# Performance work log

Measured on AMD Instinct MI355X. Metric: run time of the kernel, lower is better.

Reference implementation:

```python
import jax, jax.numpy as jnp
import numpy as np

B, S, E = 1, 4096, 2048
H, HK, D = 16, 4, 128  # num_heads, num_kv_heads, head_dim


def setup_inputs() -> dict:
    key = jax.random.key(0)
    ks = jax.random.split(key, 5)
    sc = 0.02
    return {
        "x": jax.random.normal(ks[0], (B, S, E), dtype=jnp.float32),
        "Wq": jax.random.normal(ks[1], (H * D, E), dtype=jnp.float32) * sc,
        "Wk": jax.random.normal(ks[2], (HK * D, E), dtype=jnp.float32) * sc,
        "Wv": jax.random.normal(ks[3], (HK * D, E), dtype=jnp.float32) * sc,
        "Wo": jax.random.normal(ks[4], (E, H * D), dtype=jnp.float32) * sc,
    }


def reference(x, Wq, Wk, Wv, Wo):
    b, s, _ = x.shape
    # projections (bias=False Linear: x @ W.T), split heads, [B, H, S, D]
    q = (x @ Wq.T).reshape(b, s, H, D).transpose(0, 2, 1, 3).astype(jnp.float16)
    k = (x @ Wk.T).reshape(b, s, HK, D).transpose(0, 2, 1, 3).astype(jnp.float16)
    v = (x @ Wv.T).reshape(b, s, HK, D).transpose(0, 2, 1, 3).astype(jnp.float16)
    # GQA: repeat_interleave kv heads to match query heads
    rep = H // HK
    k = jnp.repeat(k, rep, axis=1)
    v = jnp.repeat(v, rep, axis=1)
    # SDPA in fp32 (non-causal), result cast to half as in torch code
    qf, kf, vf = q.astype(jnp.float32), k.astype(jnp.float32), v.astype(jnp.float32)
    scores = jnp.einsum("bhsd,bhtd->bhst", qf, kf) / np.float32(np.sqrt(D))
    attn = jax.nn.softmax(scores, axis=-1)
    out = jnp.einsum("bhst,bhtd->bhsd", attn, vf).astype(jnp.float16)
    # merge heads and output projection in fp32
    out = out.transpose(0, 2, 1, 3).reshape(b, s, H * D).astype(jnp.float32)
    return out @ Wo.T
```

## Files before the change

### kernel.cpp

```cpp
#include <hip/hip_runtime.h>
#include <stdint.h>

#define SEQ 4096
#define EMB 2048
#define NH 16
#define HDIM 128

typedef _Float16 f16;
typedef _Float16 f16x2 __attribute__((ext_vector_type(2)));
typedef _Float16 f16x4 __attribute__((ext_vector_type(4)));
typedef _Float16 f16x8 __attribute__((ext_vector_type(8)));
typedef float f32x4 __attribute__((ext_vector_type(4)));
typedef unsigned u32x2 __attribute__((ext_vector_type(2)));

#define MFMA16(a, b, c) __builtin_amdgcn_mfma_f32_16x16x32_f16((a), (b), (c), 0, 0, 0)

#define OFF_XH   0ull
#define OFF_WCAT 8388608ull
#define OFF_WO   14680064ull
#define OFF_Q    23068672ull
#define OFF_K    31457280ull
#define OFF_VT   33554432ull

__device__ __forceinline__ void gload16(const void* g, void* l) {
    __builtin_amdgcn_global_load_lds((const __attribute__((address_space(1))) unsigned int*)g,
                                     (__attribute__((address_space(3))) unsigned int*)l, 16, 0, 0);
}

__device__ __forceinline__ void swap32p(uint32_t& x, uint32_t& y) {
#if __has_builtin(__builtin_amdgcn_permlane32_swap)
    u32x2 r = __builtin_amdgcn_permlane32_swap(x, y, false, false);
    x = r[0]; y = r[1];
#else
    int l = __lane_id();
    uint32_t xs = (uint32_t)__shfl_xor((int)x, 32, 64), ys = (uint32_t)__shfl_xor((int)y, 32, 64);
    uint32_t nx = (l < 32) ? x : ys;
    uint32_t ny = (l < 32) ? xs : y;
    x = nx; y = ny;
#endif
}
__device__ __forceinline__ void swap16p(uint32_t& x, uint32_t& y) {
#if __has_builtin(__builtin_amdgcn_permlane16_swap)
    u32x2 r = __builtin_amdgcn_permlane16_swap(x, y, false, false);
    x = r[0]; y = r[1];
#else
    int l = __lane_id();
    uint32_t xs = (uint32_t)__shfl_xor((int)x, 16, 64), ys = (uint32_t)__shfl_xor((int)y, 16, 64);
    uint32_t nx = (l & 16) ? ys : x;
    uint32_t ny = (l & 16) ? y : xs;
    x = nx; y = ny;
#endif
}
__device__ __forceinline__ float red_max_lhi(float t) {
    uint32_t a = __float_as_uint(t), b = a;
    swap16p(a, b);
    t = fmaxf(__uint_as_float(a), __uint_as_float(b));
    a = __float_as_uint(t); b = a;
    swap32p(a, b);
    return fmaxf(__uint_as_float(a), __uint_as_float(b));
}
__device__ __forceinline__ float red_sum_lhi(float t) {
    uint32_t a = __float_as_uint(t), b = a;
    swap16p(a, b);
    t = __uint_as_float(a) + __uint_as_float(b);
    a = __float_as_uint(t); b = a;
    swap32p(a, b);
    return __uint_as_float(a) + __uint_as_float(b);
}

__global__ __launch_bounds__(256) void cvt_kernel(
    const float* __restrict__ x, const float* __restrict__ wq,
    const float* __restrict__ wk, const float* __restrict__ wv,
    const float* __restrict__ wo, f16* __restrict__ ws)
{
    int g = blockIdx.x * 256 + threadIdx.x;
    const float* src;
    size_t dst;
    if (g < 2097152)      { src = x  + (size_t)g * 4;                 dst = OFF_XH + (size_t)g * 4; }
    else if (g < 3145728) { int r = g - 2097152; src = wq + (size_t)r * 4; dst = OFF_WCAT + (size_t)r * 4; }
    else if (g < 3407872) { int r = g - 3145728; src = wk + (size_t)r * 4; dst = OFF_WCAT + 4194304ull + (size_t)r * 4; }
    else if (g < 3670016) { int r = g - 3407872; src = wv + (size_t)r * 4; dst = OFF_WCAT + 5242880ull + (size_t)r * 4; }
    else                  { int r = g - 3670016; src = wo + (size_t)r * 4; dst = OFF_WO + (size_t)r * 4; }
    float4 v = *(const float4*)src;
    f16x4 hv;
    hv[0] = (f16)v.x; hv[1] = (f16)v.y; hv[2] = (f16)v.z; hv[3] = (f16)v.w;
    *(f16x4*)&ws[dst] = hv;
}

__global__ __launch_bounds__(256) void qkv_gemm(
    const f16* __restrict__ Xh, const f16* __restrict__ Wcat,
    f16* __restrict__ Qb, f16* __restrict__ Kb, f16* __restrict__ Vt)
{
    __shared__ f16 As[128 * 32];
    __shared__ f16 Bs[128 * 32];
    const int tid = threadIdx.x;
    const int lane = tid & 63;
    const int w = tid >> 6;
    const int llo = lane & 15, lhi = lane >> 4;
    const int m0 = blockIdx.y * 128;
    const int n0 = blockIdx.x * 128;
    const int wr = (w >> 1) * 64, wc = (w & 1) * 64;
    const float CS = 0.08838834764831845f * 1.4426950408889634f;

    f32x4 acc[4][4] = {};

    for (int k0 = 0; k0 < EMB; k0 += 32) {
#pragma unroll
        for (int i = 0; i < 2; ++i) {
            int c = tid + 256 * i;
            gload16(Xh + (size_t)(m0 + (c >> 2)) * EMB + k0 + (c & 3) * 8, &As[c * 8]);
        }
#pragma unroll
        for (int i = 0; i < 2; ++i) {
            int c = tid + 256 * i;
            gload16(Wcat + (size_t)(n0 + (c >> 2)) * EMB + k0 + (c & 3) * 8, &Bs[c * 8]);
        }
        __syncthreads();
        f16x8 af[4], bf[4];
#pragma unroll
        for (int mi = 0; mi < 4; ++mi) af[mi] = *(const f16x8*)&As[(wr + mi * 16 + llo) * 32 + lhi * 8];
#pragma unroll
        for (int ni = 0; ni < 4; ++ni) bf[ni] = *(const f16x8*)&Bs[(wc + ni * 16 + llo) * 32 + lhi * 8];
#pragma unroll
        for (int mi = 0; mi < 4; ++mi)
#pragma unroll
            for (int ni = 0; ni < 4; ++ni)
                acc[mi][ni] = MFMA16(af[mi], bf[ni], acc[mi][ni]);
        __syncthreads();
    }

    if (n0 < 2048) {
#pragma unroll
        for (int mi = 0; mi < 4; ++mi) {
            int m = m0 + wr + mi * 16 + lhi * 4;
#pragma unroll
            for (int ni = 0; ni < 4; ++ni) {
                int n = n0 + wc + ni * 16 + llo;
#pragma unroll
                for (int r = 0; r < 4; ++r)
                    Qb[(size_t)(m + r) * EMB + n] = (f16)(acc[mi][ni][r] * CS);
            }
        }
    } else if (n0 < 2560) {
#pragma unroll
        for (int mi = 0; mi < 4; ++mi) {
            int m = m0 + wr + mi * 16 + lhi * 4;
#pragma unroll
            for (int ni = 0; ni < 4; ++ni) {
                int n = n0 + wc + ni * 16 + llo - 2048;
#pragma unroll
                for (int r = 0; r < 4; ++r)
                    Kb[(size_t)(m + r) * 512 + n] = (f16)acc[mi][ni][r];
            }
        }
    } else {
#pragma unroll
        for (int mi = 0; mi < 4; ++mi) {
            int mb = m0 + wr + mi * 16 + lhi * 4;
#pragma unroll
            for (int ni = 0; ni < 4; ++ni) {
                int n = n0 + wc + ni * 16 + llo - 2560;
                f16x4 pv;
#pragma unroll
                for (int r = 0; r < 4; ++r) pv[r] = (f16)acc[mi][ni][r];
                *(f16x4*)&Vt[(size_t)n * SEQ + mb] = pv;
            }
        }
    }
}

__global__ __launch_bounds__(512, 4) void attn_kernel(
    const f16* __restrict__ Qb, const f16* __restrict__ Kb, const f16* __restrict__ Vt,
    f16* __restrict__ AO)
{
    __shared__ f16 Ks[2][64 * 128];
    __shared__ f16 Vs[2][128 * 64];
    const int tid = threadIdx.x, lane = tid & 63, w = tid >> 6;
    const int llo = lane & 15, lhi = lane >> 4;
    const int h = blockIdx.y, hk = h >> 2;
    const int wm0 = blockIdx.x * 128 + w * 16;
    const int hcol = h * HDIM;

    f16x8 qf[4];
#pragma unroll
    for (int kk = 0; kk < 4; ++kk)
        qf[kk] = *(const f16x8*)&Qb[(size_t)(wm0 + llo) * EMB + hcol + kk * 32 + lhi * 8];

    const f16* kgp[2];
    const f16* vgp[2];
#pragma unroll
    for (int i = 0; i < 2; ++i) {
        int c = tid + 512 * i;
        int row = c >> 4, cc = (c & 15) ^ (row & 7);
        kgp[i] = Kb + (size_t)row * 512 + hk * HDIM + cc * 8;
    }
#pragma unroll
    for (int i = 0; i < 2; ++i) {
        int c = tid + 512 * i;
        int row = c >> 3, cc = (c & 7) ^ (row & 7);
        vgp[i] = Vt + (size_t)(hk * HDIM + row) * SEQ + cc * 8;
    }

    float mrun = -3.0e38f;
    float lsum = 0.f;
    f32x4 acc[8] = {};

    auto stage = [&](int buf, int t0) {
#pragma unroll
        for (int i = 0; i < 2; ++i)
            gload16(kgp[i] + (size_t)t0 * 512, &Ks[buf][(tid + 512 * i) * 8]);
#pragma unroll
        for (int i = 0; i < 2; ++i)
            gload16(vgp[i] + t0, &Vs[buf][(tid + 512 * i) * 8]);
    };

    stage(0, 0);
    __syncthreads();

    for (int tt = 0; tt < 64; ++tt) {
        int cur = tt & 1;
        if (tt < 63) stage(cur ^ 1, (tt + 1) * 64);

        f32x4 s[4] = {};
        __builtin_amdgcn_s_setprio(1);
#pragma unroll
        for (int kk = 0; kk < 4; ++kk) {
            f16x8 kf[4];
#pragma unroll
            for (int hh = 0; hh < 4; ++hh) {
                int row = llo + 16 * hh;
                int ccs = (kk * 4 + lhi) ^ (row & 7);
                kf[hh] = *(const f16x8*)&Ks[cur][row * 128 + ccs * 8];
            }
#pragma unroll
            for (int hh = 0; hh < 4; ++hh)
                s[hh] = MFMA16(kf[hh], qf[kk], s[hh]);
        }
        __builtin_amdgcn_s_setprio(0);

        float t = -3.0e38f;
#pragma unroll
        for (int hh = 0; hh < 4; ++hh)
#pragma unroll
            for (int r = 0; r < 4; ++r) t = fmaxf(t, s[hh][r]);
        float tm = red_max_lhi(t);

        if (__any(tm > mrun + 8.f)) {
            float mnew = fmaxf(mrun, tm);
            float alpha = __builtin_amdgcn_exp2f(mrun - mnew);
            mrun = mnew; lsum *= alpha;
            float ar[4];
#pragma unroll
            for (int r = 0; r < 4; ++r) ar[r] = __shfl(alpha, lhi * 4 + r, 64);
#pragma unroll
            for (int ni = 0; ni < 8; ++ni)
#pragma unroll
                for (int r = 0; r < 4; ++r) acc[ni][r] *= ar[r];
        }

        union F2U { f16x2 h; uint32_t u; };
        uint32_t Y[4][2];
        float ts = 0.f;
#pragma unroll
        for (int hh = 0; hh < 4; ++hh) {
#pragma unroll
            for (int r = 0; r < 4; ++r) { float p = __builtin_amdgcn_exp2f(s[hh][r] - mrun); s[hh][r] = p; ts += p; }
            F2U a, b;
            a.h[0] = (f16)s[hh][0]; a.h[1] = (f16)s[hh][1];
            b.h[0] = (f16)s[hh][2]; b.h[1] = (f16)s[hh][3];
            Y[hh][0] = a.u; Y[hh][1] = b.u;
        }
        lsum += ts;

        f16x8 paf[2];
#pragma unroll
        for (int c = 0; c < 2; ++c) {
            union { f16x8 v; uint32_t u[4]; } pa;
#pragma unroll
            for (int jj = 0; jj < 2; ++jj) {
                uint32_t xa = Y[2 * c][jj], xb = Y[2 * c + 1][jj];
                swap32p(xa, xb);
                swap16p(xa, xb);
                pa.u[jj] = xa; pa.u[2 + jj] = xb;
            }
            paf[c] = pa.v;
        }

        __builtin_amdgcn_s_setprio(1);
#pragma unroll
        for (int c = 0; c < 2; ++c)
#pragma unroll
            for (int ni = 0; ni < 8; ++ni) {
                int d = ni * 16 + llo;
                f16x8 vf = *(const f16x8*)&Vs[cur][d * 64 + (((4 * c + lhi) ^ (d & 7)) * 8)];
                acc[ni] = MFMA16(paf[c], vf, acc[ni]);
            }
        __builtin_amdgcn_s_setprio(0);

        __syncthreads();
    }

    float linv = 1.0f / red_sum_lhi(lsum);
    float lr[4];
#pragma unroll
    for (int r = 0; r < 4; ++r) lr[r] = __shfl(linv, lhi * 4 + r, 64);
#pragma unroll
    for (int ni = 0; ni < 8; ++ni) {
        int n = hcol + ni * 16 + llo;
#pragma unroll
        for (int r = 0; r < 4; ++r)
            AO[(size_t)(wm0 + lhi * 4 + r) * EMB + n] = (f16)(acc[ni][r] * lr[r]);
    }
}

__global__ __launch_bounds__(256) void o_gemm(
    const f16* __restrict__ A, const f16* __restrict__ Bw,
    float* __restrict__ Co)
{
    __shared__ f16 As[128 * 32];
    __shared__ f16 Bs[128 * 32];
    const int tid = threadIdx.x;
    const int lane = tid & 63;
    const int w = tid >> 6;
    const int llo = lane & 15, lhi = lane >> 4;
    const int m0 = blockIdx.y * 128;
    const int n0 = blockIdx.x * 128;
    const int wr = (w >> 1) * 64, wc = (w & 1) * 64;

    f32x4 acc[4][4] = {};

    for (int k0 = 0; k0 < EMB; k0 += 32) {
#pragma unroll
        for (int i = 0; i < 2; ++i) {
            int c = tid + 256 * i;
            gload16(A + (size_t)(m0 + (c >> 2)) * EMB + k0 + (c & 3) * 8, &As[c * 8]);
        }
#pragma unroll
        for (int i = 0; i < 2; ++i) {
            int c = tid + 256 * i;
            gload16(Bw + (size_t)(n0 + (c >> 2)) * EMB + k0 + (c & 3) * 8, &Bs[c * 8]);
        }
        __syncthreads();
        f16x8 af[4], bf[4];
#pragma unroll
        for (int mi = 0; mi < 4; ++mi) af[mi] = *(const f16x8*)&As[(wr + mi * 16 + llo) * 32 + lhi * 8];
#pragma unroll
        for (int ni = 0; ni < 4; ++ni) bf[ni] = *(const f16x8*)&Bs[(wc + ni * 16 + llo) * 32 + lhi * 8];
#pragma unroll
        for (int mi = 0; mi < 4; ++mi)
#pragma unroll
            for (int ni = 0; ni < 4; ++ni)
                acc[mi][ni] = MFMA16(af[mi], bf[ni], acc[mi][ni]);
        __syncthreads();
    }

#pragma unroll
    for (int mi = 0; mi < 4; ++mi) {
        int m = m0 + wr + mi * 16 + lhi * 4;
#pragma unroll
        for (int ni = 0; ni < 4; ++ni) {
            int n = n0 + wc + ni * 16 + llo;
#pragma unroll
            for (int r = 0; r < 4; ++r)
                Co[(size_t)(m + r) * EMB + n] = acc[mi][ni][r];
        }
    }
}

extern "C" void kernel_launch(void* const* d_in, const int* in_sizes, int n_in,
                              void* d_out, int out_size, void* d_ws, size_t ws_size,
                              hipStream_t stream) {
    const float* x  = (const float*)d_in[0];
    const float* wq = (const float*)d_in[1];
    const float* wk = (const float*)d_in[2];
    const float* wv = (const float*)d_in[3];
    const float* wo = (const float*)d_in[4];
    f16* ws = (f16*)d_ws;

    f16* Xh   = ws + OFF_XH;
    f16* Wcat = ws + OFF_WCAT;
    f16* Wo16 = ws + OFF_WO;
    f16* Qb   = ws + OFF_Q;
    f16* Kb   = ws + OFF_K;
    f16* Vt   = ws + OFF_VT;

    cvt_kernel<<<18432, 256, 0, stream>>>(x, wq, wk, wv, wo, ws);
    qkv_gemm<<<dim3(24, 32), 256, 0, stream>>>(Xh, Wcat, Qb, Kb, Vt);
    attn_kernel<<<dim3(32, 16), 512, 0, stream>>>(Qb, Kb, Vt, Xh );
    o_gemm<<<dim3(16, 32), 256, 0, stream>>>(Xh , Wo16, (float*)d_out);
}
```

Baseline: 385.6 us.

## Rewrite attention kernel with 32x32x16 MFMA and 4 waves of 32 rows

The attention kernel moves from 16x16x32 MFMA tiles with 8 waves of 16 query rows each to 32x32x16 MFMA tiles with 4 waves of 32 query rows each. The K/V shared-memory swizzle, the softmax row reductions and the P-fragment packing are rebuilt for the 32x32 accumulator layout, using pkrtz conversion and a single permlane32 swap. The goal is fewer MFMA issues and fewer LDS fragment reads per tile, plus cheaper cross-lane reductions. The cost is a larger register footprint (Q fragments, 16-wide accumulators) and fewer waves per block, which may reduce latency hiding.

Result: no change. 389.9 us (+1.1%).

```diff
diff --git a/kernel.cpp b/kernel.cpp
--- a/kernel.cpp
+++ b/kernel.cpp
@@ -11,9 +11,11 @@
 typedef _Float16 f16x4 __attribute__((ext_vector_type(4)));
 typedef _Float16 f16x8 __attribute__((ext_vector_type(8)));
 typedef float f32x4 __attribute__((ext_vector_type(4)));
+typedef float f32x16 __attribute__((ext_vector_type(16)));
 typedef unsigned u32x2 __attribute__((ext_vector_type(2)));
 
 #define MFMA16(a, b, c) __builtin_amdgcn_mfma_f32_16x16x32_f16((a), (b), (c), 0, 0, 0)
+#define MFMA32(a, b, c) __builtin_amdgcn_mfma_f32_32x32x16_f16((a), (b), (c), 0, 0, 0)
 
 #define OFF_XH   0ull
 #define OFF_WCAT 8388608ull
@@ -39,33 +41,16 @@
     x = nx; y = ny;
 #endif
 }
-__device__ __forceinline__ void swap16p(uint32_t& x, uint32_t& y) {
-#if __has_builtin(__builtin_amdgcn_permlane16_swap)
-    u32x2 r = __builtin_amdgcn_permlane16_swap(x, y, false, false);
-    x = r[0]; y = r[1];
+
+__device__ __forceinline__ uint32_t pk2(float a, float b) {
+#if __has_builtin(__builtin_amdgcn_cvt_pkrtz)
+    typedef __fp16 h16x2 __attribute__((ext_vector_type(2)));
+    union { h16x2 h; uint32_t u; } z;
+    z.h = __builtin_amdgcn_cvt_pkrtz(a, b);
+    return z.u;
 #else
-    int l = __lane_id();
-    uint32_t xs = (uint32_t)__shfl_xor((int)x, 16, 64), ys = (uint32_t)__shfl_xor((int)y, 16, 64);
-    uint32_t nx = (l & 16) ? ys : x;
-    uint32_t ny = (l & 16) ? y : xs;
-    x = nx; y = ny;
+    union { f16x2 h; uint32_t u; } z; z.h[0] = (f16)a; z.h[1] = (f16)b; return z.u;
 #endif
-}
-__device__ __forceinline__ float red_max_lhi(float t) {
-    uint32_t a = __float_as_uint(t), b = a;
-    swap16p(a, b);
-    t = fmaxf(__uint_as_float(a), __uint_as_float(b));
-    a = __float_as_uint(t); b = a;
-    swap32p(a, b);
-    return fmaxf(__uint_as_float(a), __uint_as_float(b));
-}
-__device__ __forceinline__ float red_sum_lhi(float t) {
-    uint32_t a = __float_as_uint(t), b = a;
-    swap16p(a, b);
-    t = __uint_as_float(a) + __uint_as_float(b);
-    a = __float_as_uint(t); b = a;
-    swap32p(a, b);
-    return __uint_as_float(a) + __uint_as_float(b);
 }
 
 __global__ __launch_bounds__(256) void cvt_kernel(
@@ -169,49 +154,49 @@
     }
 }
 
-__global__ __launch_bounds__(512, 4) void attn_kernel(
+__global__ __launch_bounds__(256, 2) void attn_kernel(
     const f16* __restrict__ Qb, const f16* __restrict__ Kb, const f16* __restrict__ Vt,
     f16* __restrict__ AO)
 {
     __shared__ f16 Ks[2][64 * 128];
-    __shared__ f16 Vs[2][128 * 64];
+    __shared__ f16 Vs[2][64 * 128];
     const int tid = threadIdx.x, lane = tid & 63, w = tid >> 6;
-    const int llo = lane & 15, lhi = lane >> 4;
+    const int l31 = lane & 31, hi = lane >> 5;
     const int h = blockIdx.y, hk = h >> 2;
-    const int wm0 = blockIdx.x * 128 + w * 16;
+    const int wm0 = blockIdx.x * 128 + w * 32;
     const int hcol = h * HDIM;
-
-    f16x8 qf[4];
-#pragma unroll
-    for (int kk = 0; kk < 4; ++kk)
-        qf[kk] = *(const f16x8*)&Qb[(size_t)(wm0 + llo) * EMB + hcol + kk * 32 + lhi * 8];
-
-    const f16* kgp[2];
-    const f16* vgp[2];
-#pragma unroll
-    for (int i = 0; i < 2; ++i) {
-        int c = tid + 512 * i;
-        int row = c >> 4, cc = (c & 15) ^ (row & 7);
-        kgp[i] = Kb + (size_t)row * 512 + hk * HDIM + cc * 8;
-    }
-#pragma unroll
-    for (int i = 0; i < 2; ++i) {
-        int c = tid + 512 * i;
-        int row = c >> 3, cc = (c & 7) ^ (row & 7);
-        vgp[i] = Vt + (size_t)(hk * HDIM + row) * SEQ + cc * 8;
+    const int t15 = l31 & 15;
+    const int vrow15 = l31 >> 1;
+
+    f16x8 qf[8];
+#pragma unroll
+    for (int kk = 0; kk < 8; ++kk)
+        qf[kk] = *(const f16x8*)&Qb[(size_t)(wm0 + l31) * EMB + hcol + kk * 16 + hi * 8];
+
+    const f16* kgp[4];
+    const f16* vgp[4];
+#pragma unroll
+    for (int i = 0; i < 4; ++i) {
+        int c = tid + 256 * i;
+        int row = c >> 4, slot = c & 15;
+        int dch = slot ^ (row & 15);
+        kgp[i] = Kb + (size_t)row * 512 + hk * HDIM + dch * 8;
+        int lg = slot ^ (row & 15);
+        int d = 2 * row + (lg >> 3), tc = lg & 7;
+        vgp[i] = Vt + (size_t)(hk * HDIM + d) * SEQ + tc * 8;
     }
 
     float mrun = -3.0e38f;
     float lsum = 0.f;
-    f32x4 acc[8] = {};
+    f32x16 acc[4] = {};
 
     auto stage = [&](int buf, int t0) {
 #pragma unroll
-        for (int i = 0; i < 2; ++i)
-            gload16(kgp[i] + (size_t)t0 * 512, &Ks[buf][(tid + 512 * i) * 8]);
-#pragma unroll
-        for (int i = 0; i < 2; ++i)
-            gload16(vgp[i] + t0, &Vs[buf][(tid + 512 * i) * 8]);
+        for (int i = 0; i < 4; ++i)
+            gload16(kgp[i] + (size_t)t0 * 512, &Ks[buf][(tid + 256 * i) * 8]);
+#pragma unroll
+        for (int i = 0; i < 4; ++i)
+            gload16(vgp[i] + t0, &Vs[buf][(tid + 256 * i) * 8]);
     };
 
     stage(0, 0);
@@ -221,96 +206,103 @@
         int cur = tt & 1;
         if (tt < 63) stage(cur ^ 1, (tt + 1) * 64);
 
-        f32x4 s[4] = {};
+        f32x16 st0 = {}, st1 = {};
         __builtin_amdgcn_s_setprio(1);
 #pragma unroll
-        for (int kk = 0; kk < 4; ++kk) {
-            f16x8 kf[4];
-#pragma unroll
-            for (int hh = 0; hh < 4; ++hh) {
-                int row = llo + 16 * hh;
-                int ccs = (kk * 4 + lhi) ^ (row & 7);
-                kf[hh] = *(const f16x8*)&Ks[cur][row * 128 + ccs * 8];
-            }
-#pragma unroll
-            for (int hh = 0; hh < 4; ++hh)
-                s[hh] = MFMA16(kf[hh], qf[kk], s[hh]);
+        for (int kk = 0; kk < 8; ++kk) {
+            int slot = (kk * 2 + hi) ^ t15;
+            f16x8 kf0 = *(const f16x8*)&Ks[cur][l31 * 128 + slot * 8];
+            f16x8 kf1 = *(const f16x8*)&Ks[cur][(32 + l31) * 128 + slot * 8];
+            st0 = MFMA32(kf0, qf[kk], st0);
+            st1 = MFMA32(kf1, qf[kk], st1);
         }
         __builtin_amdgcn_s_setprio(0);
 
-        float t = -3.0e38f;
-#pragma unroll
-        for (int hh = 0; hh < 4; ++hh)
-#pragma unroll
-            for (int r = 0; r < 4; ++r) t = fmaxf(t, s[hh][r]);
-        float tm = red_max_lhi(t);
-
-        if (__any(tm > mrun + 8.f)) {
-            float mnew = fmaxf(mrun, tm);
+        float mx[8];
+#pragma unroll
+        for (int i = 0; i < 8; ++i)
+            mx[i] = fmaxf(fmaxf(st0[i], st0[i + 8]), fmaxf(st1[i], st1[i + 8]));
+#pragma unroll
+        for (int i = 0; i < 4; ++i) mx[i] = fmaxf(mx[i], mx[i + 4]);
+        float tmax = fmaxf(fmaxf(mx[0], mx[1]), fmaxf(mx[2], mx[3]));
+        {
+            uint32_t a = __float_as_uint(tmax), b = a;
+            swap32p(a, b);
+            tmax = fmaxf(__uint_as_float(a), __uint_as_float(b));
+        }
+
+        if (__any(tmax > mrun + 8.f)) {
+            float mnew = fmaxf(mrun, tmax);
             float alpha = __builtin_amdgcn_exp2f(mrun - mnew);
             mrun = mnew; lsum *= alpha;
-            float ar[4];
-#pragma unroll
-            for (int r = 0; r < 4; ++r) ar[r] = __shfl(alpha, lhi * 4 + r, 64);
-#pragma unroll
-            for (int ni = 0; ni < 8; ++ni)
-#pragma unroll
-                for (int r = 0; r < 4; ++r) acc[ni][r] *= ar[r];
-        }
-
-        union F2U { f16x2 h; uint32_t u; };
-        uint32_t Y[4][2];
+            float ar[16];
+#pragma unroll
+            for (int r = 0; r < 16; ++r)
+                ar[r] = __shfl(alpha, (r & 3) + 8 * (r >> 2) + 4 * hi, 64);
+#pragma unroll
+            for (int dt = 0; dt < 4; ++dt)
+#pragma unroll
+                for (int r = 0; r < 16; ++r) acc[dt][r] *= ar[r];
+        }
+
         float ts = 0.f;
 #pragma unroll
-        for (int hh = 0; hh < 4; ++hh) {
-#pragma unroll
-            for (int r = 0; r < 4; ++r) { float p = __builtin_amdgcn_exp2f(s[hh][r] - mrun); s[hh][r] = p; ts += p; }
-            F2U a, b;
-            a.h[0] = (f16)s[hh][0]; a.h[1] = (f16)s[hh][1];
-            b.h[0] = (f16)s[hh][2]; b.h[1] = (f16)s[hh][3];
-            Y[hh][0] = a.u; Y[hh][1] = b.u;
-        }
+        for (int r = 0; r < 16; ++r) { float p = __builtin_amdgcn_exp2f(st0[r] - mrun); st0[r] = p; ts += p; }
+#pragma unroll
+        for (int r = 0; r < 16; ++r) { float p = __builtin_amdgcn_exp2f(st1[r] - mrun); st1[r] = p; ts += p; }
         lsum += ts;
 
-        f16x8 paf[2];
-#pragma unroll
-        for (int c = 0; c < 2; ++c) {
-            union { f16x8 v; uint32_t u[4]; } pa;
-#pragma unroll
-            for (int jj = 0; jj < 2; ++jj) {
-                uint32_t xa = Y[2 * c][jj], xb = Y[2 * c + 1][jj];
-                swap32p(xa, xb);
-                swap16p(xa, xb);
-                pa.u[jj] = xa; pa.u[2 + jj] = xb;
+        f16x8 pa[4];
+#define PACKHALF(SRC, PH, KT)                                                   \
+        {                                                                       \
+            uint32_t X0 = pk2(SRC[(PH)*8 + 0], SRC[(PH)*8 + 1]);                \
+            uint32_t X1 = pk2(SRC[(PH)*8 + 2], SRC[(PH)*8 + 3]);                \
+            uint32_t X2 = pk2(SRC[(PH)*8 + 4], SRC[(PH)*8 + 5]);                \
+            uint32_t X3 = pk2(SRC[(PH)*8 + 6], SRC[(PH)*8 + 7]);                \
+            swap32p(X0, X2); swap32p(X1, X3);                                   \
+            union { f16x8 v; uint32_t u[4]; } pu;                               \
+            pu.u[0] = X0; pu.u[1] = X1; pu.u[2] = X2; pu.u[3] = X3;             \
+            pa[KT] = pu.v;                                                      \
+        }
+        PACKHALF(st0, 0, 0)
+        PACKHALF(st0, 1, 1)
+        PACKHALF(st1, 0, 2)
+        PACKHALF(st1, 1, 3)
+#undef PACKHALF
+
+        __builtin_amdgcn_s_setprio(1);
+#pragma unroll
+        for (int dt = 0; dt < 4; ++dt) {
+            int row = dt * 16 + vrow15;
+#pragma unroll
+            for (int kt = 0; kt < 4; ++kt) {
+                int slot = ((l31 & 1) * 8 + kt * 2 + hi) ^ vrow15;
+                f16x8 vf = *(const f16x8*)&Vs[cur][row * 128 + slot * 8];
+                acc[dt] = MFMA32(pa[kt], vf, acc[dt]);
             }
-            paf[c] = pa.v;
-        }
-
-        __builtin_amdgcn_s_setprio(1);
-#pragma unroll
-        for (int c = 0; c < 2; ++c)
-#pragma unroll
-            for (int ni = 0; ni < 8; ++ni) {
-                int d = ni * 16 + llo;
-                f16x8 vf = *(const f16x8*)&Vs[cur][d * 64 + (((4 * c + lhi) ^ (d & 7)) * 8)];
-                acc[ni] = MFMA16(paf[c], vf, acc[ni]);
-            }
+        }
         __builtin_amdgcn_s_setprio(0);
 
         __syncthreads();
     }
 
-    float linv = 1.0f / red_sum_lhi(lsum);
-    float lr[4];
-#pragma unroll
-    for (int r = 0; r < 4; ++r) lr[r] = __shfl(linv, lhi * 4 + r, 64);
-#pragma unroll
-    for (int ni = 0; ni < 8; ++ni) {
-        int n = hcol + ni * 16 + llo;
-#pragma unroll
-        for (int r = 0; r < 4; ++r)
-            AO[(size_t)(wm0 + lhi * 4 + r) * EMB + n] = (f16)(acc[ni][r] * lr[r]);
-    }
+    {
+        uint32_t a = __float_as_uint(lsum), b = a;
+        swap32p(a, b);
+        lsum = __uint_as_float(a) + __uint_as_float(b);
+    }
+    float linv = 1.0f / lsum;
+    float lr[16];
+#pragma unroll
+    for (int r = 0; r < 16; ++r)
+        lr[r] = __shfl(linv, (r & 3) + 8 * (r >> 2) + 4 * hi, 64);
+#pragma unroll
+    for (int dt = 0; dt < 4; ++dt)
+#pragma unroll
+        for (int r = 0; r < 16; ++r) {
+            int m = (r & 3) + 8 * (r >> 2) + 4 * hi;
+            AO[(size_t)(wm0 + m) * EMB + hcol + dt * 32 + l31] = (f16)(acc[dt][r] * lr[r]);
+        }
 }
 
 __global__ __launch_bounds__(256) void o_gemm(
@@ -386,6 +378,6 @@
 
     cvt_kernel<<<18432, 256, 0, stream>>>(x, wq, wk, wv, wo, ws);
     qkv_gemm<<<dim3(24, 32), 256, 0, stream>>>(Xh, Wcat, Qb, Kb, Vt);
-    attn_kernel<<<dim3(32, 16), 512, 0, stream>>>(Qb, Kb, Vt, Xh );
+    attn_kernel<<<dim3(32, 16), 256, 0, stream>>>(Qb, Kb, Vt, Xh );
     o_gemm<<<dim3(16, 32), 256, 0, stream>>>(Xh , Wo16, (float*)d_out);
 }
```
